# Kernel tuning notes

Hardware: AMD Instinct MI355X
Metric: run time of the kernel (lower is better)

## Reference

```python
import jax, jax.numpy as jnp
import numpy as np

N_ = 512   # batch / num users
M_ = 254   # num UAV nodes -> size S = M_ + 2 = 256
D_ = 2     # coordinate dim
H_ = 128   # pointer-net hidden dim


def setup_inputs() -> dict:
    key = jax.random.key(0)
    ks = jax.random.split(key, 7)
    s = 0.1
    return {
        "outputs": jax.random.normal(ks[0], (2 * N_ + M_, D_), dtype=jnp.float32),
        "W_embed": jax.random.normal(ks[1], (D_, H_), dtype=jnp.float32) * s,
        "b_embed": jnp.zeros((H_,), jnp.float32),
        "lstm_Wi": jax.random.normal(ks[2], (H_, 4 * H_), dtype=jnp.float32) * s,
        "lstm_Wh": jax.random.normal(ks[3], (H_, 4 * H_), dtype=jnp.float32) * s,
        "lstm_b": jnp.zeros((4 * H_,), jnp.float32),
        "att_W1": jax.random.normal(ks[4], (H_, H_), dtype=jnp.float32) * s,
        "att_W2": jax.random.normal(ks[5], (H_, H_), dtype=jnp.float32) * s,
        "att_v": jax.random.normal(ks[6], (H_,), dtype=jnp.float32) * s,
        "N": N_,
    }


def _rgnn_loss(outputs, W_embed, b_embed, lstm_Wi, lstm_Wh, lstm_b,
               att_W1, att_W2, att_v, N):
    D = outputs.shape[1]
    H = W_embed.shape[1]
    M = outputs.shape[0] - 2 * N
    users_src = outputs[:N][:, None, :]                         # (B,1,D)
    users_dst = outputs[N:2 * N][:, None, :]                    # (B,1,D)
    uav_nodes = jnp.broadcast_to(outputs[2 * N:][None, :, :], (N, M, D))
    uav_graph = jnp.concatenate([users_src, uav_nodes, users_dst], axis=1)  # (B,S,D)
    B, S = uav_graph.shape[0], uav_graph.shape[1]
    NEG = jnp.float32(-np.inf)

    # pointer-net: node embeddings and step-independent attention projection
    e_all = uav_graph @ W_embed + b_embed                       # (B,S,H)
    W1e = jnp.einsum('bsh,hk->bsk', e_all, att_W1)              # (B,S,H)
    rows = jnp.arange(B)

    mask0 = jnp.zeros((B, S), jnp.float32).at[:, 0].set(NEG)
    x0 = uav_graph[:, 0, :]                                     # start at src
    carry0 = (x0, x0,
              jnp.zeros((B, H), jnp.float32), jnp.zeros((B, H), jnp.float32),
              mask0, jnp.zeros((B,), jnp.float32))

    def step(carry, k):
        x, Y0, h, c, mask, max_dist = carry
        # dst node blocked only at step 0, re-opened afterwards
        mask = mask.at[:, -1].set(jnp.where(k == 0, NEG, 0.0))
        # LSTM cell on embedded current node
        e_x = x @ W_embed + b_embed                             # (B,H)
        gates = e_x @ lstm_Wi + h @ lstm_Wh + lstm_b            # (B,4H)
        i, f, g, o = jnp.split(gates, 4, axis=1)
        c = jax.nn.sigmoid(f) * c + jax.nn.sigmoid(i) * jnp.tanh(g)
        h = jax.nn.sigmoid(o) * jnp.tanh(c)
        # additive attention pointer logits
        q = h @ att_W2                                          # (B,H)
        logits = jnp.tanh(W1e + q[:, None, :]) @ att_v + mask   # (B,S)
        logits = jax.lax.stop_gradient(logits)                  # output.detach()
        idx = jnp.argmax(logits, axis=1)                        # (B,)
        Y1 = uav_graph[rows, idx]                               # (B,D)
        dist = jnp.sqrt(jnp.sum((Y1 - Y0) ** 2, axis=1) + 1e-12)
        max_dist = jnp.maximum(max_dist, dist)
        mask = mask.at[rows, idx].add(NEG)
        mask = jnp.where((idx == S)[:, None], NEG, mask)
        return (Y1, Y1, h, c, mask, max_dist), None

    (_, _, _, _, _, max_dist), _ = jax.lax.scan(step, carry0, jnp.arange(S))
    return max_dist.mean()


def reference(outputs, W_embed, b_embed, lstm_Wi, lstm_Wh, lstm_b,
              att_W1, att_W2, att_v, N):
    return _rgnn_loss(outputs, W_embed, b_embed, lstm_Wi, lstm_Wh, lstm_b,
                      att_W1, att_W2, att_v, N)
```

## Files before the change

kernel.cpp:

```cpp
#include <hip/hip_runtime.h>
#include <math.h>

#define NB   512
#define MM   254
#define SS   256
#define HH   128
#define RTOT 1278
#define NBLK 256

#define C2   2.885390081777927f
#define C1   1.442695040888963f

__device__ __forceinline__ float rcpf(float x)  { return __builtin_amdgcn_rcpf(x); }
__device__ __forceinline__ float exp2f_(float x){ return __builtin_amdgcn_exp2f(x); }
__device__ __forceinline__ float sigm2(float x)  { return rcpf(1.0f + exp2f_(-C1 * x)); }
__device__ __forceinline__ float tanh2(float x)  { return 1.0f - 2.0f * rcpf(1.0f + exp2f_(C2 * x)); }

__global__ __launch_bounds__(128) void precompute_k(
    const float* __restrict__ outputs, const float* __restrict__ Wemb,
    const float* __restrict__ bemb, const float* __restrict__ Wi,
    const float* __restrict__ W1, const float* __restrict__ lb,
    float4* __restrict__ EWiP, float4* __restrict__ W1eQ)
{
  int r = blockIdx.x;
  int t = threadIdx.x;
  __shared__ float e[HH];
  __shared__ float w1e[HH];
  float px = outputs[2 * r], py = outputs[2 * r + 1];
  e[t] = px * Wemb[t] + py * Wemb[HH + t] + bemb[t];
  __syncthreads();
  float acc = 0.f;
#pragma unroll 8
  for (int h = 0; h < HH; ++h) acc = fmaf(e[h], W1[h * HH + t], acc);
  w1e[t] = acc;
  float g4[4];
#pragma unroll
  for (int c = 0; c < 4; ++c) {
    int j = t + c * HH;
    float a = 0.f;
#pragma unroll 8
    for (int h = 0; h < HH; ++h) a = fmaf(e[h], Wi[h * 512 + j], a);
    g4[c] = a + lb[j];
  }
  float4 v4; v4.x = g4[0]; v4.y = g4[1]; v4.z = g4[2]; v4.w = g4[3];
  EWiP[(size_t)r * HH + t] = v4;
  __syncthreads();
  if (t < 32) {
    float4 p;
    p.x = C2 * w1e[4 * t];     p.y = C2 * w1e[4 * t + 1];
    p.z = C2 * w1e[4 * t + 2]; p.w = C2 * w1e[4 * t + 3];
    W1eQ[(size_t)t * RTOT + r] = p;
  }
}

__global__ __launch_bounds__(128) void transpose_k(
    const float* __restrict__ Wh, const float* __restrict__ W2,
    float* __restrict__ WhT, float* __restrict__ W2T)
{
  int bidx = blockIdx.x;
  int k = threadIdx.x;
  if (bidx < 512) WhT[(size_t)bidx * 128 + k] = Wh[(size_t)k * 512 + bidx];
  else {
    int j = bidx - 512;
    W2T[(size_t)j * 128 + k] = W2[(size_t)k * 128 + j];
  }
}

__global__ __attribute__((amdgpu_waves_per_eu(4, 4)))
__launch_bounds__(1024) void decode_k(
    const float* __restrict__ outputs, const float* __restrict__ WhT,
    const float* __restrict__ Wh, const float* __restrict__ W2T,
    const float* __restrict__ av,
    const float4* __restrict__ EWiP, const float4* __restrict__ W1eQ,
    float* __restrict__ maxd_out)
{
  const int t = threadIdx.x;
  const int bid = blockIdx.x;

  __shared__ float WhL[64][512];
  __shared__ float posU[2 * MM];
  __shared__ float dstS[2][2];
  __shared__ __align__(16) float hS[2][HH];
  __shared__ __align__(16) float qS[2][HH];
  __shared__ __align__(16) float vS2[HH];
  __shared__ float sumvS[2];
  __shared__ float pS[2][2][512];
  __shared__ float lp[2][2][SS];
  __shared__ int   lsS[2][SS];
  __shared__ int   actS[2][254];
  __shared__ int   cntS[2], curS[2];

  const int gh  = (t >> 5) & 1;
  const int gj  = ((t >> 6) << 5) | (t & 31);
  const int cg  = t >> 9;
  const int cj  = (t >> 2) & 127;
  const int ckq = t & 3;
  const int lg  = t >> 9;
  const int lhf = (t >> 8) & 1;
  const int lu  = t & 255;

  float4 whreg[8];
  {
    const float4* wg4 = (const float4*)(WhT + (size_t)gj * 128 + gh * 32);
#pragma unroll
    for (int i = 0; i < 8; ++i) whreg[i] = wg4[i];
  }

  for (int i = t; i < 64 * 512; i += 1024) ((float*)WhL)[i] = Wh[64 * 512 + i];
  for (int i = t; i < 2 * MM; i += 1024)   posU[i] = outputs[4 * NB + i];
  if (t < 256) { int g = t >> 7, j = t & 127; hS[g][j] = 0.f; }
  if (t < HH) vS2[t] = -2.0f * av[t];
  if (t >= 256 && t < 258) {
    int half = t - 256; float s = 0.f;
    for (int h = half * 64; h < half * 64 + 64; ++h) s += av[h];
    sumvS[half] = s;
  }
  if (t < 254) actS[0][t] = t + 1;
  else if (t >= 512 && t < 766) actS[1][t - 512] = t - 511;
  if (t == 0) {
    cntS[0] = 254; curS[0] = bid;
    dstS[0][0] = outputs[2 * (NB + bid)]; dstS[0][1] = outputs[2 * (NB + bid) + 1];
  }
  if (t == 512) {
    cntS[1] = 254; curS[1] = bid + NBLK;
    dstS[1][0] = outputs[2 * (NB + bid + NBLK)];
    dstS[1][1] = outputs[2 * (NB + bid + NBLK) + 1];
  }
  __syncthreads();

  float px = 0.f, py = 0.f, md = 0.f;
  if (t == 0)   { px = outputs[2 * bid];          py = outputs[2 * bid + 1]; }
  if (t == 512) { px = outputs[2 * (bid + NBLK)]; py = outputs[2 * (bid + NBLK) + 1]; }

  float creg = 0.f;

  for (int k = 0; k < SS; ++k) {
    float4 ew4 = make_float4(0.f, 0.f, 0.f, 0.f);
    if (t < 256) ew4 = EWiP[(size_t)curS[t >> 7] * HH + (t & 127)];
    {
      float a0G = 0.f, a1G = 0.f, a0L = 0.f, a1L = 0.f;
      {
        const float* wl = &WhL[gh * 32][gj];
        const float4* hb0 = (const float4*)(&hS[0][64 + gh * 32]);
        const float4* hb1 = (const float4*)(&hS[1][64 + gh * 32]);
#pragma unroll
        for (int i = 0; i < 8; ++i) {
          float4 h0 = hb0[i], h1 = hb1[i];
          float wa = wl[(size_t)(4 * i) * 512];
          float wbv = wl[(size_t)(4 * i + 1) * 512];
          float wc = wl[(size_t)(4 * i + 2) * 512];
          float wd = wl[(size_t)(4 * i + 3) * 512];
          a0L = fmaf(h0.x, wa, a0L); a0L = fmaf(h0.y, wbv, a0L);
          a0L = fmaf(h0.z, wc, a0L); a0L = fmaf(h0.w, wd, a0L);
          a1L = fmaf(h1.x, wa, a1L); a1L = fmaf(h1.y, wbv, a1L);
          a1L = fmaf(h1.z, wc, a1L); a1L = fmaf(h1.w, wd, a1L);
        }
      }
      {
        const float4* hb0 = (const float4*)(&hS[0][gh * 32]);
        const float4* hb1 = (const float4*)(&hS[1][gh * 32]);
#pragma unroll
        for (int i = 0; i < 8; ++i) {
          float4 h0 = hb0[i], h1 = hb1[i];
          float4 w = whreg[i];
          a0G = fmaf(h0.x, w.x, a0G); a0G = fmaf(h0.y, w.y, a0G);
          a0G = fmaf(h0.z, w.z, a0G); a0G = fmaf(h0.w, w.w, a0G);
          a1G = fmaf(h1.x, w.x, a1G); a1G = fmaf(h1.y, w.y, a1G);
          a1G = fmaf(h1.z, w.z, a1G); a1G = fmaf(h1.w, w.w, a1G);
        }
      }
      pS[0][gh][gj] = a0G + a0L;
      pS[1][gh][gj] = a1G + a1L;
    }
    __syncthreads();

    if (t < 256) {
      int g = t >> 7, jj = t & 127;
      float ei = ew4.x + (pS[g][0][jj]       + pS[g][1][jj]);
      float ef = ew4.y + (pS[g][0][128 + jj] + pS[g][1][128 + jj]);
      float eg = ew4.z + (pS[g][0][256 + jj] + pS[g][1][256 + jj]);
      float eo = ew4.w + (pS[g][0][384 + jj] + pS[g][1][384 + jj]);
      float iv = sigm2(ei), fv = sigm2(ef), gv = tanh2(eg), ov = sigm2(eo);
      float cn = fv * creg + iv * gv;
      creg = cn;
      hS[g][jj] = ov * tanh2(cn);
    }
    __syncthreads();

    {
      const float4* w4 = (const float4*)(W2T + (size_t)cj * 128 + ckq * 32);
      const float4* h4 = (const float4*)(&hS[cg][ckq * 32]);
      float p0 = 0.f, p1 = 0.f;
#pragma unroll
      for (int i = 0; i < 8; ++i) {
        float4 w = w4[i], h = h4[i];
        p0 = fmaf(h.x, w.x, p0); p1 = fmaf(h.y, w.y, p1);
        p0 = fmaf(h.z, w.z, p0); p1 = fmaf(h.w, w.w, p1);
      }
      float p = p0 + p1;
      p += __shfl_xor(p, 1);
      p += __shfl_xor(p, 2);
      if (ckq == 0) qS[cg][cj] = C2 * p;
    }
    __syncthreads();

    {
      int cnt = cntS[lg];
      int cntEff = cnt + (k > 0 ? 1 : 0);
      if (lu < cntEff) {
        int s = (lu == cnt) ? 255 : actS[lg][lu];
        int r = (s == 255) ? (NB + bid + (lg << 8)) : (2 * NB + s - 1);
        const float4* wp = W1eQ + (size_t)(lhf * 16) * RTOT + r;
        const float4* qv4 = (const float4*)(&qS[lg][lhf * 64]);
        const float4* vv4 = (const float4*)(&vS2[lhf * 64]);
        float c0 = 0.f, c1 = 0.f;
#pragma unroll 4
        for (int i = 0; i < 16; ++i) {
          float4 w = wp[(size_t)i * RTOT];
          float4 q = qv4[i];
          float4 v = vv4[i];
          c0 = fmaf(v.x, rcpf(1.0f + exp2f_(w.x + q.x)), c0);
          c1 = fmaf(v.y, rcpf(1.0f + exp2f_(w.y + q.y)), c1);
          c0 = fmaf(v.z, rcpf(1.0f + exp2f_(w.z + q.z)), c0);
          c1 = fmaf(v.w, rcpf(1.0f + exp2f_(w.w + q.w)), c1);
        }
        lp[lg][lhf][lu] = (c0 + c1) + sumvS[lhf];
        if (lhf == 0) lsS[lg][lu] = s;
      }
    }
    __syncthreads();

    if ((t < 64) || (t >= 512 && t < 576)) {
      int g = t >> 9;
      int lane = t & 63;
      int cnt = cntS[g];
      int cntEff = cnt + (k > 0 ? 1 : 0);
      float val = -INFINITY;
      unsigned key = 0xFFFFFFFFu;
#pragma unroll
      for (int c = 0; c < 4; ++c) {
        int u = lane + 64 * c;
        if (u < cntEff) {
          float v2 = lp[g][0][u] + lp[g][1][u];
          unsigned k2 = ((unsigned)lsS[g][u] << 16) | (unsigned)u;
          if (v2 > val || (v2 == val && k2 < key)) { val = v2; key = k2; }
        }
      }
#pragma unroll
      for (int off = 1; off < 64; off <<= 1) {
        float v2 = __shfl_xor(val, off);
        unsigned k2 = __shfl_xor(key, off);
        if (v2 > val || (v2 == val && k2 < key)) { val = v2; key = k2; }
      }
      if (lane == 0) {
        int s   = (int)(key >> 16);
        int pos = (int)(key & 0xFFFFu);
        int rn  = (s == 255) ? (NB + bid + (g << 8)) : (2 * NB + s - 1);
        float nx, ny;
        if (s == 255) { nx = dstS[g][0]; ny = dstS[g][1]; }
        else          { nx = posU[2 * (s - 1)]; ny = posU[2 * (s - 1) + 1]; }
        float dx = nx - px, dy = ny - py;
        float d = sqrtf(dx * dx + dy * dy + 1e-12f);
        if (d > md) md = d;
        px = nx; py = ny;
        curS[g] = rn;
        if (s != 255) { actS[g][pos] = actS[g][cnt - 1]; cntS[g] = cnt - 1; }
      }
    }
    __syncthreads();
  }

  if (t == 0)   maxd_out[bid] = md;
  if (t == 512) maxd_out[bid + NBLK] = md;
}

__global__ __launch_bounds__(512) void reduce_k(const float* __restrict__ maxd,
                                               float* __restrict__ out)
{
  __shared__ float s[512];
  int t = threadIdx.x;
  s[t] = maxd[t];
  __syncthreads();
  for (int off = 256; off > 0; off >>= 1) {
    if (t < off) s[t] += s[t + off];
    __syncthreads();
  }
  if (t == 0) out[0] = s[0] * (1.0f / 512.0f);
}

extern "C" void kernel_launch(void* const* d_in, const int* in_sizes, int n_in,
                              void* d_out, int out_size, void* d_ws, size_t ws_size,
                              hipStream_t stream) {
  const float* outputs = (const float*)d_in[0];
  const float* Wemb    = (const float*)d_in[1];
  const float* bemb    = (const float*)d_in[2];
  const float* Wi      = (const float*)d_in[3];
  const float* Wh      = (const float*)d_in[4];
  const float* lb      = (const float*)d_in[5];
  const float* W1      = (const float*)d_in[6];
  const float* W2      = (const float*)d_in[7];
  const float* av      = (const float*)d_in[8];

  float* ws    = (float*)d_ws;
  float4* EWiP = (float4*)ws;
  float4* W1eQ = (float4*)(ws + (size_t)RTOT * 512);
  float*  WhT  = ws + (size_t)RTOT * 512 + (size_t)RTOT * 128;
  float*  W2T  = WhT + (size_t)512 * 128;
  float*  maxd = W2T + (size_t)128 * 128;

  hipLaunchKernelGGL(transpose_k, dim3(640), dim3(128), 0, stream, Wh, W2, WhT, W2T);
  hipLaunchKernelGGL(precompute_k, dim3(RTOT), dim3(HH), 0, stream,
                     outputs, Wemb, bemb, Wi, W1, lb, EWiP, W1eQ);
  hipLaunchKernelGGL(decode_k, dim3(NBLK), dim3(1024), 0, stream,
                     outputs, WhT, Wh, W2T, av, EWiP, W1eQ, maxd);
  hipLaunchKernelGGL(reduce_k, dim3(1), dim3(512), 0, stream, maxd, (float*)d_out);
}
```

Before: 2.179 ms.

## Fold 2-D embedding into linear coefficients and recompute projections in-kernel

Since node embeddings are linear in 2-D coordinates, the input-gate and W1 attention projections are rewritten as px*A + py*B + C, with tiny coefficient vectors computed once by a single-block kernel. The decode kernel keeps these coefficients in shared memory and rebuilds per-node projections from coordinates, replacing the large precomputed EWiP/W1eQ tables and their scattered global loads each step. The cost is a few extra FMAs per attention element and slightly different floating-point rounding, which could flip argmax ties.

```diff
diff --git a/kernel.cpp b/kernel.cpp
--- a/kernel.cpp
+++ b/kernel.cpp
@@ -13,43 +13,34 @@
 
 __device__ __forceinline__ float rcpf(float x)  { return __builtin_amdgcn_rcpf(x); }
 __device__ __forceinline__ float exp2f_(float x){ return __builtin_amdgcn_exp2f(x); }
-__device__ __forceinline__ float sigm2(float x)  { return rcpf(1.0f + exp2f_(-C1 * x)); }
-__device__ __forceinline__ float tanh2(float x)  { return 1.0f - 2.0f * rcpf(1.0f + exp2f_(C2 * x)); }
-
-__global__ __launch_bounds__(128) void precompute_k(
-    const float* __restrict__ outputs, const float* __restrict__ Wemb,
-    const float* __restrict__ bemb, const float* __restrict__ Wi,
-    const float* __restrict__ W1, const float* __restrict__ lb,
-    float4* __restrict__ EWiP, float4* __restrict__ W1eQ)
+__device__ __forceinline__ float sigm2(float x) { return rcpf(1.0f + exp2f_(-C1 * x)); }
+__device__ __forceinline__ float tanh2(float x) { return 1.0f - 2.0f * rcpf(1.0f + exp2f_(C2 * x)); }
+
+__global__ __launch_bounds__(512) void coef_k(
+    const float* __restrict__ Wemb, const float* __restrict__ bemb,
+    const float* __restrict__ Wi, const float* __restrict__ W1,
+    const float* __restrict__ lb, float* __restrict__ coef)
 {
-  int r = blockIdx.x;
-  int t = threadIdx.x;
-  __shared__ float e[HH];
-  __shared__ float w1e[HH];
-  float px = outputs[2 * r], py = outputs[2 * r + 1];
-  e[t] = px * Wemb[t] + py * Wemb[HH + t] + bemb[t];
-  __syncthreads();
-  float acc = 0.f;
+  int j = threadIdx.x;
+  float a = 0.f, b = 0.f, c = 0.f;
 #pragma unroll 8
-  for (int h = 0; h < HH; ++h) acc = fmaf(e[h], W1[h * HH + t], acc);
-  w1e[t] = acc;
-  float g4[4];
-#pragma unroll
-  for (int c = 0; c < 4; ++c) {
-    int j = t + c * HH;
-    float a = 0.f;
+  for (int h = 0; h < HH; ++h) {
+    float w = Wi[(size_t)h * 512 + j];
+    a = fmaf(Wemb[h], w, a);
+    b = fmaf(Wemb[HH + h], w, b);
+    c = fmaf(bemb[h], w, c);
+  }
+  coef[j] = a; coef[512 + j] = b; coef[1024 + j] = c + lb[j];
+  if (j < HH) {
+    float a1 = 0.f, b1 = 0.f, c1 = 0.f;
 #pragma unroll 8
-    for (int h = 0; h < HH; ++h) a = fmaf(e[h], Wi[h * 512 + j], a);
-    g4[c] = a + lb[j];
-  }
-  float4 v4; v4.x = g4[0]; v4.y = g4[1]; v4.z = g4[2]; v4.w = g4[3];
-  EWiP[(size_t)r * HH + t] = v4;
-  __syncthreads();
-  if (t < 32) {
-    float4 p;
-    p.x = C2 * w1e[4 * t];     p.y = C2 * w1e[4 * t + 1];
-    p.z = C2 * w1e[4 * t + 2]; p.w = C2 * w1e[4 * t + 3];
-    W1eQ[(size_t)t * RTOT + r] = p;
+    for (int h = 0; h < HH; ++h) {
+      float w = W1[(size_t)h * HH + j];
+      a1 = fmaf(Wemb[h], w, a1);
+      b1 = fmaf(Wemb[HH + h], w, b1);
+      c1 = fmaf(bemb[h], w, c1);
+    }
+    coef[1536 + j] = C2 * a1; coef[1664 + j] = C2 * b1; coef[1792 + j] = C2 * c1;
   }
 }
 
@@ -70,8 +61,7 @@
 __launch_bounds__(1024) void decode_k(
     const float* __restrict__ outputs, const float* __restrict__ WhT,
     const float* __restrict__ Wh, const float* __restrict__ W2T,
-    const float* __restrict__ av,
-    const float4* __restrict__ EWiP, const float4* __restrict__ W1eQ,
+    const float* __restrict__ av, const float* __restrict__ coef,
     float* __restrict__ maxd_out)
 {
   const int t = threadIdx.x;
@@ -80,15 +70,18 @@
   __shared__ float WhL[64][512];
   __shared__ float posU[2 * MM];
   __shared__ float dstS[2][2];
+  __shared__ float curP[2][2];
   __shared__ __align__(16) float hS[2][HH];
-  __shared__ __align__(16) float qS[2][HH];
+  __shared__ __align__(16) float qC[2][HH];
   __shared__ __align__(16) float vS2[HH];
   __shared__ float sumvS[2];
+  __shared__ __align__(16) float AiS[512], BiS[512], CiS[512];
+  __shared__ __align__(16) float A1sS[HH], B1sS[HH], C1sS[HH];
   __shared__ float pS[2][2][512];
   __shared__ float lp[2][2][SS];
   __shared__ int   lsS[2][SS];
   __shared__ int   actS[2][254];
-  __shared__ int   cntS[2], curS[2];
+  __shared__ int   cntS[2];
 
   const int gh  = (t >> 5) & 1;
   const int gj  = ((t >> 6) << 5) | (t & 31);
@@ -108,7 +101,9 @@
 
   for (int i = t; i < 64 * 512; i += 1024) ((float*)WhL)[i] = Wh[64 * 512 + i];
   for (int i = t; i < 2 * MM; i += 1024)   posU[i] = outputs[4 * NB + i];
-  if (t < 256) { int g = t >> 7, j = t & 127; hS[g][j] = 0.f; }
+  if (t < 512) { AiS[t] = coef[t]; BiS[t] = coef[512 + t]; CiS[t] = coef[1024 + t]; }
+  if (t < HH)  { A1sS[t] = coef[1536 + t]; B1sS[t] = coef[1664 + t]; C1sS[t] = coef[1792 + t]; }
+  if (t < 256) { int gg = t >> 7, j = t & 127; hS[gg][j] = 0.f; }
   if (t < HH) vS2[t] = -2.0f * av[t];
   if (t >= 256 && t < 258) {
     int half = t - 256; float s = 0.f;
@@ -118,25 +113,26 @@
   if (t < 254) actS[0][t] = t + 1;
   else if (t >= 512 && t < 766) actS[1][t - 512] = t - 511;
   if (t == 0) {
-    cntS[0] = 254; curS[0] = bid;
+    cntS[0] = 254;
     dstS[0][0] = outputs[2 * (NB + bid)]; dstS[0][1] = outputs[2 * (NB + bid) + 1];
+    curP[0][0] = outputs[2 * bid];        curP[0][1] = outputs[2 * bid + 1];
   }
   if (t == 512) {
-    cntS[1] = 254; curS[1] = bid + NBLK;
+    cntS[1] = 254;
     dstS[1][0] = outputs[2 * (NB + bid + NBLK)];
     dstS[1][1] = outputs[2 * (NB + bid + NBLK) + 1];
+    curP[1][0] = outputs[2 * (bid + NBLK)];
+    curP[1][1] = outputs[2 * (bid + NBLK) + 1];
   }
   __syncthreads();
 
   float px = 0.f, py = 0.f, md = 0.f;
-  if (t == 0)   { px = outputs[2 * bid];          py = outputs[2 * bid + 1]; }
-  if (t == 512) { px = outputs[2 * (bid + NBLK)]; py = outputs[2 * (bid + NBLK) + 1]; }
+  if (t == 0)   { px = curP[0][0]; py = curP[0][1]; }
+  if (t == 512) { px = curP[1][0]; py = curP[1][1]; }
 
   float creg = 0.f;
 
   for (int k = 0; k < SS; ++k) {
-    float4 ew4 = make_float4(0.f, 0.f, 0.f, 0.f);
-    if (t < 256) ew4 = EWiP[(size_t)curS[t >> 7] * HH + (t & 127)];
     {
       float a0G = 0.f, a1G = 0.f, a0L = 0.f, a1L = 0.f;
       {
@@ -176,10 +172,11 @@
 
     if (t < 256) {
       int g = t >> 7, jj = t & 127;
-      float ei = ew4.x + (pS[g][0][jj]       + pS[g][1][jj]);
-      float ef = ew4.y + (pS[g][0][128 + jj] + pS[g][1][128 + jj]);
-      float eg = ew4.z + (pS[g][0][256 + jj] + pS[g][1][256 + jj]);
-      float eo = ew4.w + (pS[g][0][384 + jj] + pS[g][1][384 + jj]);
+      float pxc = curP[g][0], pyc = curP[g][1];
+      float ei = fmaf(pxc, AiS[jj],       fmaf(pyc, BiS[jj],       CiS[jj]))       + (pS[g][0][jj]       + pS[g][1][jj]);
+      float ef = fmaf(pxc, AiS[128 + jj], fmaf(pyc, BiS[128 + jj], CiS[128 + jj])) + (pS[g][0][128 + jj] + pS[g][1][128 + jj]);
+      float eg = fmaf(pxc, AiS[256 + jj], fmaf(pyc, BiS[256 + jj], CiS[256 + jj])) + (pS[g][0][256 + jj] + pS[g][1][256 + jj]);
+      float eo = fmaf(pxc, AiS[384 + jj], fmaf(pyc, BiS[384 + jj], CiS[384 + jj])) + (pS[g][0][384 + jj] + pS[g][1][384 + jj]);
       float iv = sigm2(ei), fv = sigm2(ef), gv = tanh2(eg), ov = sigm2(eo);
       float cn = fv * creg + iv * gv;
       creg = cn;
@@ -200,7 +197,7 @@
       float p = p0 + p1;
       p += __shfl_xor(p, 1);
       p += __shfl_xor(p, 2);
-      if (ckq == 0) qS[cg][cj] = C2 * p;
+      if (ckq == 0) qC[cg][cj] = fmaf(C2, p, C1sS[cj]);
     }
     __syncthreads();
 
@@ -209,20 +206,25 @@
       int cntEff = cnt + (k > 0 ? 1 : 0);
       if (lu < cntEff) {
         int s = (lu == cnt) ? 255 : actS[lg][lu];
-        int r = (s == 255) ? (NB + bid + (lg << 8)) : (2 * NB + s - 1);
-        const float4* wp = W1eQ + (size_t)(lhf * 16) * RTOT + r;
-        const float4* qv4 = (const float4*)(&qS[lg][lhf * 64]);
+        float pxn, pyn;
+        if (s == 255) { pxn = dstS[lg][0]; pyn = dstS[lg][1]; }
+        else          { pxn = posU[2 * (s - 1)]; pyn = posU[2 * (s - 1) + 1]; }
+        const float4* a14 = (const float4*)(&A1sS[lhf * 64]);
+        const float4* b14 = (const float4*)(&B1sS[lhf * 64]);
+        const float4* qc4 = (const float4*)(&qC[lg][lhf * 64]);
         const float4* vv4 = (const float4*)(&vS2[lhf * 64]);
         float c0 = 0.f, c1 = 0.f;
 #pragma unroll 4
         for (int i = 0; i < 16; ++i) {
-          float4 w = wp[(size_t)i * RTOT];
-          float4 q = qv4[i];
-          float4 v = vv4[i];
-          c0 = fmaf(v.x, rcpf(1.0f + exp2f_(w.x + q.x)), c0);
-          c1 = fmaf(v.y, rcpf(1.0f + exp2f_(w.y + q.y)), c1);
-          c0 = fmaf(v.z, rcpf(1.0f + exp2f_(w.z + q.z)), c0);
-          c1 = fmaf(v.w, rcpf(1.0f + exp2f_(w.w + q.w)), c1);
+          float4 a = a14[i], b = b14[i], qc = qc4[i], v = vv4[i];
+          float wx = fmaf(pxn, a.x, fmaf(pyn, b.x, qc.x));
+          float wy = fmaf(pxn, a.y, fmaf(pyn, b.y, qc.y));
+          float wz = fmaf(pxn, a.z, fmaf(pyn, b.z, qc.z));
+          float ww = fmaf(pxn, a.w, fmaf(pyn, b.w, qc.w));
+          c0 = fmaf(v.x, rcpf(1.0f + exp2f_(wx)), c0);
+          c1 = fmaf(v.y, rcpf(1.0f + exp2f_(wy)), c1);
+          c0 = fmaf(v.z, rcpf(1.0f + exp2f_(wz)), c0);
+          c1 = fmaf(v.w, rcpf(1.0f + exp2f_(ww)), c1);
         }
         lp[lg][lhf][lu] = (c0 + c1) + sumvS[lhf];
         if (lhf == 0) lsS[lg][lu] = s;
@@ -255,7 +257,6 @@
       if (lane == 0) {
         int s   = (int)(key >> 16);
         int pos = (int)(key & 0xFFFFu);
-        int rn  = (s == 255) ? (NB + bid + (g << 8)) : (2 * NB + s - 1);
         float nx, ny;
         if (s == 255) { nx = dstS[g][0]; ny = dstS[g][1]; }
         else          { nx = posU[2 * (s - 1)]; ny = posU[2 * (s - 1) + 1]; }
@@ -263,7 +264,7 @@
         float d = sqrtf(dx * dx + dy * dy + 1e-12f);
         if (d > md) md = d;
         px = nx; py = ny;
-        curS[g] = rn;
+        curP[g][0] = nx; curP[g][1] = ny;
         if (s != 255) { actS[g][pos] = actS[g][cnt - 1]; cntS[g] = cnt - 1; }
       }
     }
@@ -301,17 +302,16 @@
   const float* W2      = (const float*)d_in[7];
   const float* av      = (const float*)d_in[8];
 
-  float* ws    = (float*)d_ws;
-  float4* EWiP = (float4*)ws;
-  float4* W1eQ = (float4*)(ws + (size_t)RTOT * 512);
-  float*  WhT  = ws + (size_t)RTOT * 512 + (size_t)RTOT * 128;
-  float*  W2T  = WhT + (size_t)512 * 128;
-  float*  maxd = W2T + (size_t)128 * 128;
-
+  float* ws   = (float*)d_ws;
+  float* coef = ws;
+  float* WhT  = coef + 2048;
+  float* W2T  = WhT + (size_t)512 * 128;
+  float* maxd = W2T + (size_t)128 * 128;
+
+  hipLaunchKernelGGL(coef_k, dim3(1), dim3(512), 0, stream,
+                     Wemb, bemb, Wi, W1, lb, coef);
   hipLaunchKernelGGL(transpose_k, dim3(640), dim3(128), 0, stream, Wh, W2, WhT, W2T);
-  hipLaunchKernelGGL(precompute_k, dim3(RTOT), dim3(HH), 0, stream,
-                     outputs, Wemb, bemb, Wi, W1, lb, EWiP, W1eQ);
   hipLaunchKernelGGL(decode_k, dim3(NBLK), dim3(1024), 0, stream,
-                     outputs, WhT, Wh, W2T, av, EWiP, W1eQ, maxd);
+                     outputs, WhT, Wh, W2T, av, coef, maxd);
   hipLaunchKernelGGL(reduce_k, dim3(1), dim3(512), 0, stream, maxd, (float*)d_out);
 }
```

Result: faster. 2.121 ms (-2.6%).
